# Kernel tuning notes

Hardware: AMD Instinct MI355X
Metric: run time of the kernel (lower is better)

## Reference

```python
import jax, jax.numpy as jnp
import numpy as np

D_MODEL = 1024
D = 512
B = 32
L = 1024


def setup_inputs() -> dict:
    key = jax.random.key(0)
    ks = jax.random.split(key, 8)
    s = 1.0 / np.sqrt(D_MODEL)
    x = jax.random.normal(ks[0], (B, L, D_MODEL), dtype=jnp.float32)
    mask = jnp.ones((B, 1, L), dtype=jnp.int32)  # padding mask; 1 = keep
    Wq = jax.random.uniform(ks[1], (D, D_MODEL), jnp.float32, -s, s)
    bq = jax.random.uniform(ks[2], (D,), jnp.float32, -s, s)
    Wk = jax.random.uniform(ks[3], (D, D_MODEL), jnp.float32, -s, s)
    bk = jax.random.uniform(ks[4], (D,), jnp.float32, -s, s)
    Wv = jax.random.uniform(ks[5], (D, D_MODEL), jnp.float32, -s, s)
    bv = jax.random.uniform(ks[6], (D,), jnp.float32, -s, s)
    return {"x": x, "Wq": Wq, "bq": bq, "Wk": Wk, "bk": bk, "Wv": Wv, "bv": bv, "mask": mask}


def reference(x, Wq, bq, Wk, bk, Wv, bv, mask):
    Bq, Lq, _ = x.shape
    q = jnp.einsum('blc,dc->bld', x, Wq) + bq  # [B,L,D]
    k = jnp.einsum('blc,dc->bld', x, Wk) + bk
    v = jnp.einsum('blc,dc->bld', x, Wv) + bv
    scale = k.shape[-1] ** -0.5
    weights = jnp.einsum('bid,bjd->bij', q, k) * scale  # [B,L,L]
    causal = jnp.tril(jnp.ones((Lq, Lq), dtype=bool))
    neg_inf = jnp.float32(-jnp.inf)
    weights = jnp.where(causal[None, :, :], weights, neg_inf)
    weights = jnp.where(mask == 0, neg_inf, weights)  # mask broadcasts [B,1,L]
    weights = jax.nn.softmax(weights, axis=-1)
    # NOTE: source calls self.dropout(weights) but discards result -> no-op
    out = jnp.einsum('bij,bjd->bid', weights, v)
    return jax.nn.relu(out)
```

## Files before the change

### kernel.cpp

```cpp
#include <hip/hip_runtime.h>
#include <hip/hip_bf16.h>
#include <stdint.h>

#define DM 1024
#define DD 512
#define BB 32
#define LL 1024
#define SCALE 0.04419417382415922f
#define MAT ((size_t)BB * LL * DD)

typedef float f32x4 __attribute__((ext_vector_type(4)));
typedef short bf16x8 __attribute__((ext_vector_type(8)));
typedef short bf16x4 __attribute__((ext_vector_type(4)));

__device__ inline unsigned short f2bf(float f) {
    union { float f; uint32_t u; } v; v.f = f;
    uint32_t r = v.u + 0x7fffu + ((v.u >> 16) & 1u);
    return (unsigned short)(r >> 16);
}
__device__ inline float bf2f(unsigned short u) {
    union { uint32_t u; float f; } v; v.u = ((uint32_t)u) << 16;
    return v.f;
}

__device__ inline bf16x4 cvt4(f32x4 a, float s) {
    bf16x4 r;
    r[0] = (short)f2bf(a[0] * s);
    r[1] = (short)f2bf(a[1] * s);
    r[2] = (short)f2bf(a[2] * s);
    r[3] = (short)f2bf(a[3] * s);
    return r;
}

#define GLOAD_LDS16(gsrc, ldst) \
    __builtin_amdgcn_global_load_lds((const __attribute__((address_space(1))) unsigned int*)(gsrc), \
        (__attribute__((address_space(3))) unsigned int*)(ldst), 16, 0, 0)

__device__ inline void publish_barrier() {
    asm volatile("s_waitcnt vmcnt(0)" ::: "memory");
    __builtin_amdgcn_sched_barrier(0);
    __builtin_amdgcn_s_barrier();
    __builtin_amdgcn_sched_barrier(0);
}
__device__ inline void gate4() {
    asm volatile("s_waitcnt vmcnt(4)" ::: "memory");
    __builtin_amdgcn_sched_barrier(0);
    __builtin_amdgcn_s_barrier();
    __builtin_amdgcn_sched_barrier(0);
}
__device__ inline void gate2() {
    asm volatile("s_waitcnt vmcnt(2)" ::: "memory");
    __builtin_amdgcn_sched_barrier(0);
    __builtin_amdgcn_s_barrier();
    __builtin_amdgcn_sched_barrier(0);
}
__device__ inline void gate0() {
    asm volatile("s_waitcnt vmcnt(0)" ::: "memory");
    __builtin_amdgcn_sched_barrier(0);
    __builtin_amdgcn_s_barrier();
    __builtin_amdgcn_sched_barrier(0);
}
__device__ inline void gateB() {
    __builtin_amdgcn_sched_barrier(0);
    __builtin_amdgcn_s_barrier();
    __builtin_amdgcn_sched_barrier(0);
}

__global__ __launch_bounds__(256) void cast_all(const float* __restrict__ x,
                                                const float* __restrict__ Wq,
                                                const float* __restrict__ Wk,
                                                const float* __restrict__ Wv,
                                                unsigned short* __restrict__ xb,
                                                unsigned short* __restrict__ Wb)
{
    int bx = blockIdx.x;
    if (bx < 16384) {
        size_t idx = (size_t)bx * 256 + threadIdx.x;
        size_t base = idx * 8;
        f32x4 a = *(const f32x4*)(x + base);
        f32x4 b = *(const f32x4*)(x + base + 4);
        bf16x4 lo = cvt4(a, 1.0f), hi = cvt4(b, 1.0f);
        bf16x8 o = {lo[0], lo[1], lo[2], lo[3], hi[0], hi[1], hi[2], hi[3]};
        *(bf16x8*)(xb + base) = o;
    } else {
        size_t idx = (size_t)(bx - 16384) * 256 + threadIdx.x;
        int o = (int)(idx >> 16);
        size_t rem = idx & 65535;
        const float* W = (o == 0) ? Wq : (o == 1) ? Wk : Wv;
        float s = (o == 0) ? SCALE : 1.0f;
        size_t base = rem * 8;
        f32x4 a = *(const f32x4*)(W + base);
        f32x4 b = *(const f32x4*)(W + base + 4);
        bf16x4 lo = cvt4(a, s), hi = cvt4(b, s);
        bf16x8 out = {lo[0], lo[1], lo[2], lo[3], hi[0], hi[1], hi[2], hi[3]};
        *(bf16x8*)(Wb + (size_t)o * 524288 + base) = out;
    }
}

__global__ __launch_bounds__(512, 2) void qkv_proj6(
    const unsigned short* __restrict__ xb,
    const unsigned short* __restrict__ Wb,
    const float* __restrict__ bq, const float* __restrict__ bk, const float* __restrict__ bv,
    unsigned short* __restrict__ qkv,
    unsigned short* __restrict__ vt)
{
    __shared__ __align__(16) unsigned short AL[2][2][8192];
    __shared__ __align__(16) unsigned short BL[2][2][8192];

    const int o = blockIdx.y;
    const float* bias = (o == 0) ? bq : (o == 1) ? bk : bv;
    const float wscale = (o == 0) ? SCALE : 1.0f;
    const unsigned short* W = Wb + (size_t)o * 524288;
    unsigned short* out = qkv + (size_t)o * MAT;

    int wg = blockIdx.x;
    wg = (wg & 7) * 32 + (wg >> 3);
    const int mt = wg >> 1, nt = wg & 1;
    const int rowbase = mt * 256;
    const int colbase = nt * 256;

    const int tid  = threadIdx.x;
    const int lane = tid & 63;
    const int w    = tid >> 6;
    const int wm   = w >> 2;
    const int wn   = w & 3;
    const int l15  = lane & 15, l4 = lane >> 4;
    const int rxor = l15 & 7;

    const int r8   = lane >> 3;
    const int swch = (lane & 7) ^ r8;

    const char* xpanel = (const char*)(xb + (size_t)rowbase * DM);
    const char* wpanel = (const char*)(W  + (size_t)colbase * DM);

    #define STAGE_HALF(panel, T, H, slot) do {                                   \
        _Pragma("unroll")                                                        \
        for (int i2 = 0; i2 < 2; ++i2) {                                         \
            int grp = i2 * 8 + w;                                                \
            GLOAD_LDS16((panel) + ((size_t)((H) * 128 + grp * 8 + r8) * 2048)    \
                            + (size_t)(T) * 128 + swch * 16,                     \
                        (char*)(slot) + grp * 1024);                             \
        }                                                                        \
    } while (0)

    #define RDA(base, mf4, ks) (*(const bf16x8*)((base) + (wm * 64 + (mf4) * 16 + l15) * 128 \
                            + ((((ks) * 4 + l4) ^ rxor) << 4)))
    #define RDB(base, nfl, ks) (*(const bf16x8*)((base) + (wn * 32 + (nfl) * 16 + l15) * 128 \
                            + ((((ks) * 4 + l4) ^ rxor) << 4)))

    f32x4 acc[8][4];
    #pragma unroll
    for (int i = 0; i < 8; ++i)
        #pragma unroll
        for (int j = 0; j < 4; ++j)
            acc[i][j] = (f32x4){0.f, 0.f, 0.f, 0.f};

    bf16x8 aF[4][2], bF[4][2];

    STAGE_HALF(xpanel, 0, 0, &AL[0][0][0]);
    STAGE_HALF(wpanel, 0, 0, &BL[0][0][0]);
    STAGE_HALF(wpanel, 0, 1, &BL[0][1][0]);
    STAGE_HALF(xpanel, 0, 1, &AL[0][1][0]);

    for (int t = 0; t < 16; ++t) {
        const int c = t & 1, cn = c ^ 1;
        const char* A0b = (const char*)&AL[c][0][0];
        const char* A1b = (const char*)&AL[c][1][0];
        const char* B0b = (const char*)&BL[c][0][0];
        const char* B1b = (const char*)&BL[c][1][0];
        const bool st = (t < 15);

        if (st) { STAGE_HALF(xpanel, t + 1, 0, &AL[cn][0][0]); gate4(); } else gate2();
        #pragma unroll
        for (int ks = 0; ks < 2; ++ks) {
            #pragma unroll
            for (int mf = 0; mf < 4; ++mf) aF[mf][ks] = RDA(A0b, mf, ks);
            bF[0][ks] = RDB(B0b, 0, ks);
            bF[1][ks] = RDB(B0b, 1, ks);
        }
        #pragma unroll
        for (int ks = 0; ks < 2; ++ks) {
            bF[2][ks] = RDB(B1b, 0, ks);
            bF[3][ks] = RDB(B1b, 1, ks);
        }
        #pragma unroll
        for (int ks = 0; ks < 2; ++ks)
            #pragma unroll
            for (int nf = 0; nf < 2; ++nf)
                #pragma unroll
                for (int mf = 0; mf < 4; ++mf)
                    acc[mf][nf] = __builtin_amdgcn_mfma_f32_16x16x32_bf16(aF[mf][ks], bF[nf][ks], acc[mf][nf], 0, 0, 0);

        if (st) { STAGE_HALF(wpanel, t + 1, 0, &BL[cn][0][0]); gate4(); } else gate0();
        #pragma unroll
        for (int ks = 0; ks < 2; ++ks)
            #pragma unroll
            for (int nf = 0; nf < 2; ++nf)
                #pragma unroll
                for (int mf = 0; mf < 4; ++mf)
                    acc[mf][2 + nf] = __builtin_amdgcn_mfma_f32_16x16x32_bf16(aF[mf][ks], bF[2 + nf][ks], acc[mf][2 + nf], 0, 0, 0);
        #pragma unroll
        for (int ks = 0; ks < 2; ++ks)
            #pragma unroll
            for (int mf = 0; mf < 4; ++mf) aF[mf][ks] = RDA(A1b, mf, ks);

        if (st) STAGE_HALF(wpanel, t + 1, 1, &BL[cn][1][0]);
        gateB();
        #pragma unroll
        for (int ks = 0; ks < 2; ++ks)
            #pragma unroll
            for (int nf = 0; nf < 2; ++nf)
                #pragma unroll
                for (int mf = 0; mf < 4; ++mf)
                    acc[4 + mf][nf] = __builtin_amdgcn_mfma_f32_16x16x32_bf16(aF[mf][ks], bF[nf][ks], acc[4 + mf][nf], 0, 0, 0);

        if (st) STAGE_HALF(xpanel, t + 1, 1, &AL[cn][1][0]);
        gateB();
        #pragma unroll
        for (int ks = 0; ks < 2; ++ks)
            #pragma unroll
            for (int nf = 0; nf < 2; ++nf)
                #pragma unroll
                for (int mf = 0; mf < 4; ++mf)
                    acc[4 + mf][2 + nf] = __builtin_amdgcn_mfma_f32_16x16x32_bf16(aF[mf][ks], bF[2 + nf][ks], acc[4 + mf][2 + nf], 0, 0, 0);
    }
    #undef STAGE_HALF
    #undef RDA
    #undef RDB

    if (o != 2) {
        #pragma unroll
        for (int nf = 0; nf < 4; ++nf) {
            int col = colbase + ((nf < 2) ? wn * 32 + nf * 16 : 128 + wn * 32 + (nf - 2) * 16) + l15;
            float bv_ = bias[col] * wscale;
            #pragma unroll
            for (int mf = 0; mf < 8; ++mf) {
                int row0 = rowbase + ((mf < 4) ? wm * 64 + mf * 16 : 128 + wm * 64 + (mf - 4) * 16) + l4 * 4;
                #pragma unroll
                for (int r = 0; r < 4; ++r)
                    out[(size_t)(row0 + r) * DD + col] = f2bf(acc[mf][nf][r] + bv_);
            }
        }
    } else {
        unsigned short* ldsT = (unsigned short*)&AL[0][0][0];
        const int bidx  = rowbase >> 10;
        const int lbase = rowbase & 1023;
        #pragma unroll
        for (int p = 0; p < 4; ++p) {
            __syncthreads();
            #pragma unroll
            for (int nf = 0; nf < 4; ++nf) {
                int base16 = (nf < 2) ? wn * 32 + nf * 16 : 128 + wn * 32 + (nf - 2) * 16;
                if (base16 >= p * 64 && base16 < p * 64 + 64) {
                    int cc = base16 - p * 64 + l15;
                    float bv_ = bias[colbase + base16 + l15];
                    #pragma unroll
                    for (int mf = 0; mf < 8; ++mf) {
                        int rowl = ((mf < 4) ? wm * 64 + mf * 16 : 128 + wm * 64 + (mf - 4) * 16) + l4 * 4;
                        bf16x4 v4;
                        #pragma unroll
                        for (int r = 0; r < 4; ++r)
                            v4[r] = (short)f2bf(acc[mf][nf][r] + bv_);
                        *(bf16x4*)&ldsT[cc * 264 + rowl] = v4;
                    }
                }
            }
            __syncthreads();
            #pragma unroll
            for (int it = 0; it < 4; ++it) {
                int uu = tid + it * 512;
                int cc = uu >> 5;
                int r0 = (uu & 31) * 8;
                bf16x8 val = *(const bf16x8*)&ldsT[cc * 264 + r0];
                int dg = colbase + p * 64 + cc;
                *(bf16x8*)(vt + ((size_t)(bidx * DD + dg)) * LL + lbase + r0) = val;
            }
        }
    }
}

__global__ __launch_bounds__(256, 2) void sgemm_qk(
    const unsigned short* __restrict__ qkv,
    unsigned short* __restrict__ S)
{
    __shared__ __align__(16) unsigned short At[2][8192];
    __shared__ __align__(16) unsigned short Bt[2][8192];

    int wg = blockIdx.x;
    wg = (wg & 7) * 144 + (wg >> 3);
    const int b = wg / 36;
    const int t36 = wg % 36;
    int mt = 0, accq = 0;
    while (accq + mt + 1 <= t36) { ++mt; accq += mt; }
    const int nt = t36 - accq;

    const int tid  = threadIdx.x;
    const int lane = tid & 63;
    const int w    = tid >> 6;
    const int wr   = (w >> 1) * 64;
    const int wc   = (w & 1) * 64;
    const int l15  = lane & 15, l4 = lane >> 4;

    const int r8   = lane >> 3;
    const int swch = (lane & 7) ^ r8;

    const unsigned short* q = qkv;
    const unsigned short* k = qkv + MAT;
    const char* apanel = (const char*)(q + ((size_t)(b * LL) + mt * 128) * DD);
    const char* bpanel = (const char*)(k + ((size_t)(b * LL) + nt * 128) * DD);

    f32x4 acc[4][4];
    #pragma unroll
    for (int i = 0; i < 4; ++i)
        #pragma unroll
        for (int j = 0; j < 4; ++j)
            acc[i][j] = (f32x4){0.f, 0.f, 0.f, 0.f};

    #define STAGE_QK(KK, BUF) do {                                               \
        _Pragma("unroll")                                                        \
        for (int i2 = 0; i2 < 4; ++i2) {                                         \
            int grp = i2 * 4 + w;                                                \
            size_t rowoff = (size_t)(grp * 8 + r8) * 1024 + (KK) * 2 + swch * 16;\
            GLOAD_LDS16(apanel + rowoff, (char*)&At[BUF][0] + grp * 1024);       \
            GLOAD_LDS16(bpanel + rowoff, (char*)&Bt[BUF][0] + grp * 1024);       \
        }                                                                        \
    } while (0)

    STAGE_QK(0, 0);
    __syncthreads();

    for (int t = 0; t < 8; ++t) {
        const int cur = t & 1;
        if (t < 7) STAGE_QK((t + 1) * 64, cur ^ 1);

        const char* Ab = (const char*)&At[cur][0];
        const char* Bb = (const char*)&Bt[cur][0];
        #pragma unroll
        for (int ks = 0; ks < 2; ++ks) {
            bf16x8 af[4], bf_[4];
            const int ch = (ks * 4 + l4) ^ (l15 & 7);
            #pragma unroll
            for (int m = 0; m < 4; ++m)
                af[m] = *(const bf16x8*)(Ab + (wr + m * 16 + l15) * 128 + (ch << 4));
            #pragma unroll
            for (int n = 0; n < 4; ++n)
                bf_[n] = *(const bf16x8*)(Bb + (wc + n * 16 + l15) * 128 + (ch << 4));
            #pragma unroll
            for (int n = 0; n < 4; ++n)
                #pragma unroll
                for (int m = 0; m < 4; ++m)
                    acc[m][n] = __builtin_amdgcn_mfma_f32_16x16x32_bf16(af[m], bf_[n], acc[m][n], 0, 0, 0);
        }

        if (t < 7) publish_barrier();
    }
    #undef STAGE_QK

    unsigned short* sp = S + ((size_t)(b * LL) + mt * 128) * LL + nt * 128;
    #pragma unroll
    for (int n = 0; n < 4; ++n) {
        int col = wc + n * 16 + l15;
        #pragma unroll
        for (int m = 0; m < 4; ++m) {
            int row0 = wr + m * 16 + l4 * 4;
            #pragma unroll
            for (int r = 0; r < 4; ++r)
                sp[(size_t)(row0 + r) * LL + col] = f2bf(acc[m][n][r]);
        }
    }
}

__global__ __launch_bounds__(256) void softmax_rows(
    const unsigned short* __restrict__ S,
    const int* __restrict__ mask,
    unsigned short* __restrict__ P)
{
    __shared__ float mbias[1024];
    const int rc = blockIdx.x, b = blockIdx.y;
    const int tid = threadIdx.x, lane = tid & 63, w = tid >> 6;

    {
        const int* mp = mask + b * LL;
        #pragma unroll
        for (int j = 0; j < 4; ++j)
            mbias[tid * 4 + j] = mp[tid * 4 + j] ? 0.0f : -1e30f;
    }
    __syncthreads();

    const int j0 = lane * 16;
    const int limit = ((rc >> 2) + 1) << 7;
    for (int i = 0; i < 8; ++i) {
        const int r = rc * 32 + i * 4 + w;
        const unsigned short* srow = S + ((size_t)(b * LL) + r) * LL;

        bf16x8 v0 = {0,0,0,0,0,0,0,0}, v1 = {0,0,0,0,0,0,0,0};
        if (j0 <= r)     v0 = *(const bf16x8*)(srow + j0);
        if (j0 + 8 <= r) v1 = *(const bf16x8*)(srow + j0 + 8);

        float s[16];
        #pragma unroll
        for (int e = 0; e < 8; ++e) {
            int j = j0 + e;
            s[e]     = (j <= r)     ? bf2f((unsigned short)v0[e]) + mbias[j]     : -3e38f;
            s[8 + e] = (j + 8 <= r) ? bf2f((unsigned short)v1[e]) + mbias[j + 8] : -3e38f;
        }
        float mx = s[0];
        #pragma unroll
        for (int e = 1; e < 16; ++e) mx = fmaxf(mx, s[e]);
        mx = fmaxf(mx, __shfl_xor(mx, 1));
        mx = fmaxf(mx, __shfl_xor(mx, 2));
        mx = fmaxf(mx, __shfl_xor(mx, 4));
        mx = fmaxf(mx, __shfl_xor(mx, 8));
        mx = fmaxf(mx, __shfl_xor(mx, 16));
        mx = fmaxf(mx, __shfl_xor(mx, 32));

        float p[16], ls = 0.f;
        #pragma unroll
        for (int e = 0; e < 16; ++e) { p[e] = __expf(s[e] - mx); ls += p[e]; }
        ls += __shfl_xor(ls, 1);
        ls += __shfl_xor(ls, 2);
        ls += __shfl_xor(ls, 4);
        ls += __shfl_xor(ls, 8);
        ls += __shfl_xor(ls, 16);
        ls += __shfl_xor(ls, 32);
        const float inv = 1.0f / ls;

        if (j0 < limit) {
            bf16x8 o0, o1;
            #pragma unroll
            for (int e = 0; e < 8; ++e) {
                o0[e] = (short)f2bf(p[e] * inv);
                o1[e] = (short)f2bf(p[8 + e] * inv);
            }
            unsigned short* prow = P + ((size_t)(b * LL) + r) * LL;
            *(bf16x8*)(prow + j0)     = o0;
            *(bf16x8*)(prow + j0 + 8) = o1;
        }
    }
}

__global__ __launch_bounds__(256, 2) void pv_gemm(
    const unsigned short* __restrict__ P,
    const unsigned short* __restrict__ vt,
    float* __restrict__ outp)
{
    __shared__ __align__(16) unsigned short At[2][8192];
    __shared__ __align__(16) unsigned short Bt[2][8192];

    int wg = blockIdx.x;
    wg = (wg & 7) * 128 + (wg >> 3);
    const int b  = wg >> 5;
    const int rr = wg & 31;
    const int rt = 7 - (rr >> 2);
    const int ct = rr & 3;

    const int tid  = threadIdx.x;
    const int lane = tid & 63;
    const int w    = tid >> 6;
    const int wr   = (w >> 1) * 64;
    const int wc   = (w & 1) * 64;
    const int l15  = lane & 15, l4 = lane >> 4;

    const int r8   = lane >> 3;
    const int swch = (lane & 7) ^ r8;

    const char* apanel = (const char*)(P  + ((size_t)(b * LL) + rt * 128) * LL);
    const char* bpanel = (const char*)(vt + ((size_t)(b * DD) + ct * 128) * LL);

    const int NT = (rt + 1) * 2;

    f32x4 acc[4][4];
    #pragma unroll
    for (int i = 0; i < 4; ++i)
        #pragma unroll
        for (int j = 0; j < 4; ++j)
            acc[i][j] = (f32x4){0.f, 0.f, 0.f, 0.f};

    #define STAGE_PV(KK, BUF) do {                                               \
        _Pragma("unroll")                                                        \
        for (int i2 = 0; i2 < 4; ++i2) {                                         \
            int grp = i2 * 4 + w;                                                \
            size_t rowoff = (size_t)(grp * 8 + r8) * 2048 + (KK) * 2 + swch * 16;\
            GLOAD_LDS16(apanel + rowoff, (char*)&At[BUF][0] + grp * 1024);       \
            GLOAD_LDS16(bpanel + rowoff, (char*)&Bt[BUF][0] + grp * 1024);       \
        }                                                                        \
    } while (0)

    STAGE_PV(0, 0);
    __syncthreads();

    for (int t = 0; t < NT; ++t) {
        const int cur = t & 1;
        if (t < NT - 1) STAGE_PV((t + 1) * 64, cur ^ 1);

        const char* Ab = (const char*)&At[cur][0];
        const char* Bb = (const char*)&Bt[cur][0];
        #pragma unroll
        for (int ks = 0; ks < 2; ++ks) {
            bf16x8 af[4], bf_[4];
            const int ch = (ks * 4 + l4) ^ (l15 & 7);
            #pragma unroll
            for (int m = 0; m < 4; ++m)
                af[m] = *(const bf16x8*)(Ab + (wr + m * 16 + l15) * 128 + (ch << 4));
            #pragma unroll
            for (int n = 0; n < 4; ++n)
                bf_[n] = *(const bf16x8*)(Bb + (wc + n * 16 + l15) * 128 + (ch << 4));
            #pragma unroll
            for (int n = 0; n < 4; ++n)
                #pragma unroll
                for (int m = 0; m < 4; ++m)
                    acc[m][n] = __builtin_amdgcn_mfma_f32_16x16x32_bf16(af[m], bf_[n], acc[m][n], 0, 0, 0);
        }

        if (t < NT - 1) publish_barrier();
    }
    #undef STAGE_PV

    float* op = outp + ((size_t)(b * LL) + rt * 128) * DD + ct * 128;
    #pragma unroll
    for (int n = 0; n < 4; ++n) {
        int col = wc + n * 16 + l15;
        #pragma unroll
        for (int m = 0; m < 4; ++m) {
            int row0 = wr + m * 16 + l4 * 4;
            #pragma unroll
            for (int r = 0; r < 4; ++r)
                op[(size_t)(row0 + r) * DD + col] = fmaxf(acc[m][n][r], 0.f);
        }
    }
}

extern "C" void kernel_launch(void* const* d_in, const int* in_sizes, int n_in,
                              void* d_out, int out_size, void* d_ws, size_t ws_size,
                              hipStream_t stream) {
    const float* x  = (const float*)d_in[0];
    const float* Wq = (const float*)d_in[1];
    const float* bq = (const float*)d_in[2];
    const float* Wk = (const float*)d_in[3];
    const float* bk = (const float*)d_in[4];
    const float* Wv = (const float*)d_in[5];
    const float* bv = (const float*)d_in[6];
    const int* mask = (const int*)d_in[7];

    unsigned short* qkv = (unsigned short*)d_ws;
    unsigned short* vtp = qkv + 2 * MAT;
    unsigned short* Wb  = qkv + 3 * MAT;
    unsigned short* xb  = (unsigned short*)d_out;
    unsigned short* S   = (unsigned short*)d_out;
    unsigned short* Pp  = qkv;
    float* out = (float*)d_out;

    cast_all<<<17152, 256, 0, stream>>>(x, Wq, Wk, Wv, xb, Wb);
    qkv_proj6<<<dim3(256, 3), 512, 0, stream>>>(xb, Wb, bq, bk, bv, qkv, vtp);
    sgemm_qk<<<dim3(1152), 256, 0, stream>>>(qkv, S);
    softmax_rows<<<dim3(32, 32), 256, 0, stream>>>(S, mask, Pp);
    pv_gemm<<<dim3(1024), 256, 0, stream>>>(Pp, vtp, out);
}
```

Before: 243.6 us.

## Fuse x fp32-to-bf16 cast into QKV projection A-tile loading

Drops the separate pass that converts x to bf16. The projection kernel now reads x in fp32 into registers, converts it and writes the A tile into LDS itself, while B tiles still use direct global-to-LDS loads. This avoids writing and re-reading a 64MB bf16 copy of x. In exchange x is read in fp32 three times (once per Q/K/V grid row), register pressure rises, and the pipeline barriers are restructured with full vmcnt/lgkmcnt waits.

After: 282.9 us. 1.16x slower.

```diff
diff --git a/kernel.cpp b/kernel.cpp
--- a/kernel.cpp
+++ b/kernel.cpp
@@ -42,63 +42,42 @@
     __builtin_amdgcn_s_barrier();
     __builtin_amdgcn_sched_barrier(0);
 }
-__device__ inline void gate4() {
+__device__ inline void gateB() {
+    __builtin_amdgcn_sched_barrier(0);
+    __builtin_amdgcn_s_barrier();
+    __builtin_amdgcn_sched_barrier(0);
+}
+__device__ inline void gate0L() {
+    asm volatile("s_waitcnt vmcnt(0) lgkmcnt(0)" ::: "memory");
+    __builtin_amdgcn_sched_barrier(0);
+    __builtin_amdgcn_s_barrier();
+    __builtin_amdgcn_sched_barrier(0);
+}
+__device__ inline void waitA() {
     asm volatile("s_waitcnt vmcnt(4)" ::: "memory");
     __builtin_amdgcn_sched_barrier(0);
-    __builtin_amdgcn_s_barrier();
-    __builtin_amdgcn_sched_barrier(0);
-}
-__device__ inline void gate2() {
-    asm volatile("s_waitcnt vmcnt(2)" ::: "memory");
-    __builtin_amdgcn_sched_barrier(0);
-    __builtin_amdgcn_s_barrier();
-    __builtin_amdgcn_sched_barrier(0);
-}
-__device__ inline void gate0() {
-    asm volatile("s_waitcnt vmcnt(0)" ::: "memory");
-    __builtin_amdgcn_sched_barrier(0);
-    __builtin_amdgcn_s_barrier();
-    __builtin_amdgcn_sched_barrier(0);
-}
-__device__ inline void gateB() {
-    __builtin_amdgcn_sched_barrier(0);
-    __builtin_amdgcn_s_barrier();
-    __builtin_amdgcn_sched_barrier(0);
-}
-
-__global__ __launch_bounds__(256) void cast_all(const float* __restrict__ x,
-                                                const float* __restrict__ Wq,
-                                                const float* __restrict__ Wk,
-                                                const float* __restrict__ Wv,
-                                                unsigned short* __restrict__ xb,
-                                                unsigned short* __restrict__ Wb)
+}
+
+__global__ __launch_bounds__(256) void cast_w(const float* __restrict__ Wq,
+                                              const float* __restrict__ Wk,
+                                              const float* __restrict__ Wv,
+                                              unsigned short* __restrict__ Wb)
 {
-    int bx = blockIdx.x;
-    if (bx < 16384) {
-        size_t idx = (size_t)bx * 256 + threadIdx.x;
-        size_t base = idx * 8;
-        f32x4 a = *(const f32x4*)(x + base);
-        f32x4 b = *(const f32x4*)(x + base + 4);
-        bf16x4 lo = cvt4(a, 1.0f), hi = cvt4(b, 1.0f);
-        bf16x8 o = {lo[0], lo[1], lo[2], lo[3], hi[0], hi[1], hi[2], hi[3]};
-        *(bf16x8*)(xb + base) = o;
-    } else {
-        size_t idx = (size_t)(bx - 16384) * 256 + threadIdx.x;
-        int o = (int)(idx >> 16);
-        size_t rem = idx & 65535;
-        const float* W = (o == 0) ? Wq : (o == 1) ? Wk : Wv;
-        float s = (o == 0) ? SCALE : 1.0f;
-        size_t base = rem * 8;
-        f32x4 a = *(const f32x4*)(W + base);
-        f32x4 b = *(const f32x4*)(W + base + 4);
-        bf16x4 lo = cvt4(a, s), hi = cvt4(b, s);
-        bf16x8 out = {lo[0], lo[1], lo[2], lo[3], hi[0], hi[1], hi[2], hi[3]};
-        *(bf16x8*)(Wb + (size_t)o * 524288 + base) = out;
-    }
-}
-
-__global__ __launch_bounds__(512, 2) void qkv_proj6(
-    const unsigned short* __restrict__ xb,
+    size_t idx = (size_t)blockIdx.x * 256 + threadIdx.x;
+    int o = (int)(idx >> 16);
+    size_t rem = idx & 65535;
+    const float* W = (o == 0) ? Wq : (o == 1) ? Wk : Wv;
+    float s = (o == 0) ? SCALE : 1.0f;
+    size_t base = rem * 8;
+    f32x4 a = *(const f32x4*)(W + base);
+    f32x4 b = *(const f32x4*)(W + base + 4);
+    bf16x4 lo = cvt4(a, s), hi = cvt4(b, s);
+    bf16x8 out = {lo[0], lo[1], lo[2], lo[3], hi[0], hi[1], hi[2], hi[3]};
+    *(bf16x8*)(Wb + (size_t)o * 524288 + base) = out;
+}
+
+__global__ __launch_bounds__(512, 2) void qkv_proj7(
+    const float* __restrict__ xf,
     const unsigned short* __restrict__ Wb,
     const float* __restrict__ bq, const float* __restrict__ bk, const float* __restrict__ bv,
     unsigned short* __restrict__ qkv,
@@ -130,19 +109,47 @@
     const int r8   = lane >> 3;
     const int swch = (lane & 7) ^ r8;
 
-    const char* xpanel = (const char*)(xb + (size_t)rowbase * DM);
-    const char* wpanel = (const char*)(W  + (size_t)colbase * DM);
-
-    #define STAGE_HALF(panel, T, H, slot) do {                                   \
+    const char* xpanelf = (const char*)(xf + (size_t)rowbase * DM);
+    const char* wpanel  = (const char*)(W  + (size_t)colbase * DM);
+
+    #define STAGE_B(T, H, slot) do {                                             \
         _Pragma("unroll")                                                        \
         for (int i2 = 0; i2 < 2; ++i2) {                                         \
             int grp = i2 * 8 + w;                                                \
-            GLOAD_LDS16((panel) + ((size_t)((H) * 128 + grp * 8 + r8) * 2048)    \
+            GLOAD_LDS16(wpanel + ((size_t)((H) * 128 + grp * 8 + r8) * 2048)     \
                             + (size_t)(T) * 128 + swch * 16,                     \
                         (char*)(slot) + grp * 1024);                             \
         }                                                                        \
     } while (0)
 
+    #define LOAD_A(T) do {                                                       \
+        _Pragma("unroll")                                                        \
+        for (int H = 0; H < 2; ++H)                                              \
+            _Pragma("unroll")                                                    \
+            for (int i2 = 0; i2 < 2; ++i2) {                                     \
+                int grp = i2 * 8 + w;                                            \
+                const char* src = xpanelf                                        \
+                    + ((size_t)(H * 128 + grp * 8 + r8) * 4096)                  \
+                    + (size_t)(T) * 256 + swch * 32;                             \
+                av[H * 4 + i2 * 2]     = *(const f32x4*)(src);                   \
+                av[H * 4 + i2 * 2 + 1] = *(const f32x4*)(src + 16);              \
+            }                                                                    \
+    } while (0)
+
+    #define CVT_WRITE_A(BUF) do {                                                \
+        _Pragma("unroll")                                                        \
+        for (int H = 0; H < 2; ++H)                                              \
+            _Pragma("unroll")                                                    \
+            for (int i2 = 0; i2 < 2; ++i2) {                                     \
+                int grp = i2 * 8 + w;                                            \
+                bf16x4 lo = cvt4(av[H * 4 + i2 * 2], 1.0f);                      \
+                bf16x4 hi = cvt4(av[H * 4 + i2 * 2 + 1], 1.0f);                  \
+                bf16x8 ov = {lo[0], lo[1], lo[2], lo[3],                         \
+                             hi[0], hi[1], hi[2], hi[3]};                        \
+                *(bf16x8*)((char*)&AL[BUF][H][0] + grp * 1024 + lane * 16) = ov; \
+            }                                                                    \
+    } while (0)
+
     #define RDA(base, mf4, ks) (*(const bf16x8*)((base) + (wm * 64 + (mf4) * 16 + l15) * 128 \
                             + ((((ks) * 4 + l4) ^ rxor) << 4)))
     #define RDB(base, nfl, ks) (*(const bf16x8*)((base) + (wn * 32 + (nfl) * 16 + l15) * 128 \
@@ -156,11 +163,14 @@
             acc[i][j] = (f32x4){0.f, 0.f, 0.f, 0.f};
 
     bf16x8 aF[4][2], bF[4][2];
-
-    STAGE_HALF(xpanel, 0, 0, &AL[0][0][0]);
-    STAGE_HALF(wpanel, 0, 0, &BL[0][0][0]);
-    STAGE_HALF(wpanel, 0, 1, &BL[0][1][0]);
-    STAGE_HALF(xpanel, 0, 1, &AL[0][1][0]);
+    f32x4 av[8];
+
+    LOAD_A(0);
+    STAGE_B(0, 0, &BL[0][0][0]);
+    STAGE_B(0, 1, &BL[0][1][0]);
+    waitA();
+    CVT_WRITE_A(0);
+    __syncthreads();
 
     for (int t = 0; t < 16; ++t) {
         const int c = t & 1, cn = c ^ 1;
@@ -170,7 +180,8 @@
         const char* B1b = (const char*)&BL[c][1][0];
         const bool st = (t < 15);
 
-        if (st) { STAGE_HALF(xpanel, t + 1, 0, &AL[cn][0][0]); gate4(); } else gate2();
+        gate0L();
+        if (st) LOAD_A(t + 1);
         #pragma unroll
         for (int ks = 0; ks < 2; ++ks) {
             #pragma unroll
@@ -191,7 +202,8 @@
                 for (int mf = 0; mf < 4; ++mf)
                     acc[mf][nf] = __builtin_amdgcn_mfma_f32_16x16x32_bf16(aF[mf][ks], bF[nf][ks], acc[mf][nf], 0, 0, 0);
 
-        if (st) { STAGE_HALF(wpanel, t + 1, 0, &BL[cn][0][0]); gate4(); } else gate0();
+        gateB();
+        if (st) STAGE_B(t + 1, 0, &BL[cn][0][0]);
         #pragma unroll
         for (int ks = 0; ks < 2; ++ks)
             #pragma unroll
@@ -204,8 +216,8 @@
             #pragma unroll
             for (int mf = 0; mf < 4; ++mf) aF[mf][ks] = RDA(A1b, mf, ks);
 
-        if (st) STAGE_HALF(wpanel, t + 1, 1, &BL[cn][1][0]);
         gateB();
+        if (st) STAGE_B(t + 1, 1, &BL[cn][1][0]);
         #pragma unroll
         for (int ks = 0; ks < 2; ++ks)
             #pragma unroll
@@ -214,8 +226,8 @@
                 for (int mf = 0; mf < 4; ++mf)
                     acc[4 + mf][nf] = __builtin_amdgcn_mfma_f32_16x16x32_bf16(aF[mf][ks], bF[nf][ks], acc[4 + mf][nf], 0, 0, 0);
 
-        if (st) STAGE_HALF(xpanel, t + 1, 1, &AL[cn][1][0]);
         gateB();
+        if (st) { waitA(); CVT_WRITE_A(cn); }
         #pragma unroll
         for (int ks = 0; ks < 2; ++ks)
             #pragma unroll
@@ -224,7 +236,9 @@
                 for (int mf = 0; mf < 4; ++mf)
                     acc[4 + mf][2 + nf] = __builtin_amdgcn_mfma_f32_16x16x32_bf16(aF[mf][ks], bF[2 + nf][ks], acc[4 + mf][2 + nf], 0, 0, 0);
     }
-    #undef STAGE_HALF
+    #undef STAGE_B
+    #undef LOAD_A
+    #undef CVT_WRITE_A
     #undef RDA
     #undef RDB
 
@@ -545,13 +559,12 @@
     unsigned short* qkv = (unsigned short*)d_ws;
     unsigned short* vtp = qkv + 2 * MAT;
     unsigned short* Wb  = qkv + 3 * MAT;
-    unsigned short* xb  = (unsigned short*)d_out;
     unsigned short* S   = (unsigned short*)d_out;
     unsigned short* Pp  = qkv;
     float* out = (float*)d_out;
 
-    cast_all<<<17152, 256, 0, stream>>>(x, Wq, Wk, Wv, xb, Wb);
-    qkv_proj6<<<dim3(256, 3), 512, 0, stream>>>(xb, Wb, bq, bk, bv, qkv, vtp);
+    cast_w<<<768, 256, 0, stream>>>(Wq, Wk, Wv, Wb);
+    qkv_proj7<<<dim3(256, 3), 512, 0, stream>>>(x, Wb, bq, bk, bv, qkv, vtp);
     sgemm_qk<<<dim3(1152), 256, 0, stream>>>(qkv, S);
     softmax_rows<<<dim3(32, 32), 256, 0, stream>>>(S, mask, Pp);
     pv_gemm<<<dim3(1024), 256, 0, stream>>>(Pp, vtp, out);
```
